# Kernel tuning notes

Measured on AMD Instinct MI355X. Metric: run time of the kernel, lower is better.

The kernel has to match this reference:

```python
import jax, jax.numpy as jnp
import numpy as np


def setup_inputs() -> dict:
    key = jax.random.key(0)
    kq, kk, kv = jax.random.split(key, 3)
    B, S, H, HK, D = 2, 2048, 32, 8, 128
    q = jax.random.normal(kq, (B, S, H, D), dtype=jnp.float32)
    k = jax.random.normal(kk, (B, S, HK, D), dtype=jnp.float32)
    v = jax.random.normal(kv, (B, S, HK, D), dtype=jnp.float32)
    return {"q": q, "k": k, "v": v}


def reference(q, k, v):
    # Causal grouped-query attention (the math vLLM's paged attention computes
    # for a full prefill where the KV cache holds exactly this sequence).
    B, S, H, D = q.shape
    HK = k.shape[2]
    G = H // HK  # query heads per kv head
    scale = jnp.asarray(D, q.dtype) ** -0.5
    qg = q.reshape(B, S, HK, G, D)
    # scores: [B, HK, G, S(q), S(k)]
    scores = jnp.einsum("bshgd,bthd->bhgst", qg, k) * scale
    causal = jnp.tril(jnp.ones((S, S), dtype=bool))  # [Sq, Sk]
    scores = jnp.where(causal, scores, jnp.finfo(scores.dtype).min)
    probs = jax.nn.softmax(scores, axis=-1)
    out = jnp.einsum("bhgst,bthd->bshgd", probs, v)  # [B, S, HK, G, D]
    return out.reshape(B, S, H * D)
```

## Files before the change

kernel.cpp:

```cpp
#include <hip/hip_runtime.h>
#include <hip/hip_bf16.h>

typedef __attribute__((ext_vector_type(8))) short short8;
typedef __attribute__((ext_vector_type(4))) short short4v;
typedef __attribute__((ext_vector_type(4))) float f32x4;
typedef __attribute__((ext_vector_type(16))) float f32x16;

#define MFMA32(a,b,c) __builtin_amdgcn_mfma_f32_32x32x16_bf16(a,b,c,0,0,0)

static __device__ __forceinline__ short f2bf(float f){
    union{float f;unsigned u;}x; x.f=f;
    unsigned r=(x.u+0x7FFFu+((x.u>>16)&1u))>>16;
    return (short)r;
}

static __device__ __forceinline__ unsigned pkbf(float lo, float hi){
    unsigned r;
    asm("v_cvt_pk_bf16_f32 %0, %1, %2" : "=v"(r) : "v"(lo), "v"(hi));
    return r;
}

static __device__ __forceinline__ void gl_lds16(const void* g, void* l){
    __builtin_amdgcn_global_load_lds(
        (const __attribute__((address_space(1))) unsigned int*)g,
        (__attribute__((address_space(3))) unsigned int*)l, 16, 0, 0);
}

static __device__ __forceinline__ short8 pfrag(int hi,
        float e0,float e1,float e2,float e3,
        float e4,float e5,float e6,float e7){
    unsigned a01 = pkbf(e0,e1), a23 = pkbf(e2,e3);
    unsigned a45 = pkbf(e4,e5), a67 = pkbf(e6,e7);
    unsigned b01 = __shfl_xor(a01, 32);
    unsigned b23 = __shfl_xor(a23, 32);
    unsigned b45 = __shfl_xor(a45, 32);
    unsigned b67 = __shfl_xor(a67, 32);
    union{ unsigned u[4]; short8 s; } w;
    w.u[0] = hi ? b45 : a01;
    w.u[1] = hi ? b67 : a23;
    w.u[2] = hi ? a45 : b01;
    w.u[3] = hi ? a67 : b23;
    return w.s;
}

constexpr int S_=2048, H_=32, HK_=8, D_=128;
constexpr int KVBLK=64;

__global__ __launch_bounds__(256) void prep(const float* __restrict__ k, const float* __restrict__ v,
                                            short* __restrict__ kb, short* __restrict__ vt){
    __shared__ short tile[64*65];
    int bid = blockIdx.x;
    if (bid < 4096){
        int t = bid*256 + threadIdx.x;
        int e = t*4;
        int d  = e & 127;
        int hk = (e>>7) & 7;
        int s  = (e>>10) & 2047;
        int b  = e>>21;
        f32x4 x = *(const f32x4*)(k + ((size_t)((b*S_+s)*HK_+hk))*D_ + d);
        short4v o;
        o[0]=f2bf(x[0]); o[1]=f2bf(x[1]); o[2]=f2bf(x[2]); o[3]=f2bf(x[3]);
        *(short4v*)(kb + ((size_t)((b*HK_+hk)*S_+s))*D_ + d) = o;
    } else {
        bid -= 4096;
        int d0 = (bid & 1)*64;
        int s0 = ((bid>>1) & 31)*64;
        int hk = (bid>>6) & 7;
        int b  = bid>>9;
        int tid = threadIdx.x;
        #pragma unroll
        for(int i=0;i<4;i++){
            int idx = i*1024 + tid*4;
            int r = idx>>6, c = idx&63;
            f32x4 x = *(const f32x4*)(v + ((size_t)((b*S_+s0+r)*HK_+hk))*D_ + d0 + c);
            tile[(c+0)*65 + r] = f2bf(x[0]);
            tile[(c+1)*65 + r] = f2bf(x[1]);
            tile[(c+2)*65 + r] = f2bf(x[2]);
            tile[(c+3)*65 + r] = f2bf(x[3]);
        }
        __syncthreads();
        #pragma unroll
        for(int i=0;i<4;i++){
            int idx = i*1024 + tid*4;
            int dr = idx>>6, c = idx&63;
            short4v o;
            o[0]=tile[dr*65+c]; o[1]=tile[dr*65+c+1]; o[2]=tile[dr*65+c+2]; o[3]=tile[dr*65+c+3];
            *(short4v*)(vt + ((size_t)((b*HK_+hk)*D_ + d0+dr))*S_ + s0 + c) = o;
        }
    }
}

__global__ __launch_bounds__(256,2) void attn_fwd(
    const float* __restrict__ q, const short* __restrict__ kb,
    const short* __restrict__ vtb, float* __restrict__ out)
{
    __shared__ __align__(16) unsigned char kls[KVBLK*D_*2];
    __shared__ __align__(16) unsigned char vls[D_*KVBLK*2];

    const int bid  = blockIdx.x;
    const int s    = bid >> 8;
    const int j    = bid & 255;
    const int xcd  = j & 7;
    const int t    = j >> 3;
    const int kvg  = xcd*2 + (t & 1);
    const int u    = t >> 1;
    const int hsub = u & 3;
    const int cq   = u >> 2;
    int c;
    switch(s){ case 0: c = 15-cq; break; case 1: c = 8+cq; break;
               case 2: c = 7-cq;  break; default: c = cq; }
    const int b    = kvg >> 3;
    const int hk   = kvg & 7;
    const int h    = hk*4 + hsub;
    const int q0   = c * 128;

    const int tid  = threadIdx.x;
    const int wave = tid >> 6;
    const int ln   = tid & 31;
    const int hi   = (tid >> 5) & 1;
    const int qg   = q0 + wave*32 + ln;

    const float qscale = 0.08838834764831845f * 1.4426950408889634f;

    const short* kt_base = kb  + (size_t)(b*HK_+hk)*S_*D_;
    const short* vt_base = vtb + (size_t)(b*HK_+hk)*D_*S_;

    short8 qf[8];
    {
        const float* qp = q + ((size_t)(b*S_ + qg)*H_ + h)*D_;
        #pragma unroll
        for(int kk=0;kk<8;kk++){
            int d0 = kk*16 + hi*8;
            f32x4 a = *(const f32x4*)(qp + d0);
            f32x4 cc= *(const f32x4*)(qp + d0 + 4);
            union{ unsigned u[4]; short8 s; } w;
            w.u[0]=pkbf(a[0]*qscale, a[1]*qscale);
            w.u[1]=pkbf(a[2]*qscale, a[3]*qscale);
            w.u[2]=pkbf(cc[0]*qscale, cc[1]*qscale);
            w.u[3]=pkbf(cc[2]*qscale, cc[3]*qscale);
            qf[kk]=w.s;
        }
    }

    f32x16 oac[4];
    #pragma unroll
    for(int dt=0;dt<4;dt++) oac[dt] = (f32x16)0.f;
    float m = -1e30f, l = 0.f;

    auto STAGE = [&](int kvt){
        const char* kg = (const char*)(kt_base + (size_t)kvt*KVBLK*D_);
        #pragma unroll
        for(int i=0;i<4;i++){
            int pp = (i*256 + tid)*16;
            int src = pp ^ (((pp>>8)&7)<<4);
            gl_lds16(kg + src, &kls[pp]);
        }
        const char* vg = (const char*)vt_base + (size_t)kvt*KVBLK*2;
        #pragma unroll
        for(int i=0;i<4;i++){
            int pp = (i*256 + tid)*16;
            int d = pp>>7;
            int src = (pp&127) ^ ((d&7)<<4);
            gl_lds16(vg + (size_t)d*(S_*2) + src, &vls[pp]);
        }
    };

    const int nkv    = 2*c + 2;
    const int kvmaxw = 2*c + (wave >> 1);

    for(int kvt=0; kvt<nkv; ++kvt){
        if (kvt) __syncthreads();
        STAGE(kvt);
        __syncthreads();

        if (kvt <= kvmaxw){
            const int kv0 = kvt*64;
            f32x16 sa0=(f32x16)0.f, sa1=(f32x16)0.f;
            const int sz = (ln&7)<<4;
            __builtin_amdgcn_s_setprio(1);
            #pragma unroll
            for(int kk=0;kk<8;kk++){
                int cb = kk*32 + hi*16;
                short8 k0 = *(const short8*)&kls[(ln*256 + cb) ^ sz];
                short8 k1 = *(const short8*)&kls[((ln+32)*256 + cb) ^ sz];
                sa0 = MFMA32(k0, qf[kk], sa0);
                sa1 = MFMA32(k1, qf[kk], sa1);
            }
            __builtin_amdgcn_s_setprio(0);
            if (kv0 + 63 > q0 + wave*32){
                #pragma unroll
                for(int r=0;r<16;r++){
                    int kvl = (r&3) + 8*(r>>2) + 4*hi;
                    if (kv0 + kvl      > qg) sa0[r] = -1e30f;
                    if (kv0 + 32 + kvl > qg) sa1[r] = -1e30f;
                }
            }
            float pm = sa0[0];
            #pragma unroll
            for(int r=1;r<16;r++) pm = fmaxf(pm, sa0[r]);
            #pragma unroll
            for(int r=0;r<16;r++) pm = fmaxf(pm, sa1[r]);
            pm = fmaxf(pm, __shfl_xor(pm, 32));
            if (!__all(pm <= m + 8.f)){
                float mn = fmaxf(m, pm);
                float sf = __builtin_amdgcn_exp2f(m - mn);
                m = mn; l *= sf;
                #pragma unroll
                for(int dt=0;dt<4;dt++){
                    #pragma unroll
                    for(int r=0;r<16;r++) oac[dt][r] *= sf;
                }
            }
            float ps = 0.f;
            #pragma unroll
            for(int r=0;r<16;r++){ sa0[r] = __builtin_amdgcn_exp2f(sa0[r]-m); ps += sa0[r]; }
            #pragma unroll
            for(int r=0;r<16;r++){ sa1[r] = __builtin_amdgcn_exp2f(sa1[r]-m); ps += sa1[r]; }
            l += ps + __shfl_xor(ps, 32);
            short8 pa0 = pfrag(hi, sa0[0],sa0[1],sa0[2], sa0[3], sa0[4], sa0[5], sa0[6], sa0[7]);
            short8 pa1 = pfrag(hi, sa0[8],sa0[9],sa0[10],sa0[11],sa0[12],sa0[13],sa0[14],sa0[15]);
            short8 pa2 = pfrag(hi, sa1[0],sa1[1],sa1[2], sa1[3], sa1[4], sa1[5], sa1[6], sa1[7]);
            short8 pa3 = pfrag(hi, sa1[8],sa1[9],sa1[10],sa1[11],sa1[12],sa1[13],sa1[14],sa1[15]);
            __builtin_amdgcn_s_setprio(1);
            #pragma unroll
            for(int dt=0;dt<4;dt++){
                int rb = (dt*32 + ln)*128;
                short8 v0 = *(const short8*)&vls[(rb +   0 + hi*16) ^ sz];
                oac[dt] = MFMA32(v0, pa0, oac[dt]);
                short8 v1 = *(const short8*)&vls[(rb +  32 + hi*16) ^ sz];
                oac[dt] = MFMA32(v1, pa1, oac[dt]);
                short8 v2 = *(const short8*)&vls[(rb +  64 + hi*16) ^ sz];
                oac[dt] = MFMA32(v2, pa2, oac[dt]);
                short8 v3 = *(const short8*)&vls[(rb +  96 + hi*16) ^ sz];
                oac[dt] = MFMA32(v3, pa3, oac[dt]);
            }
            __builtin_amdgcn_s_setprio(0);
        }
    }

    float rinv = 1.0f / l;
    float* op = out + ((size_t)(b*S_ + qg)*H_ + h)*D_;
    #pragma unroll
    for(int dt=0;dt<4;dt++){
        #pragma unroll
        for(int rr=0;rr<4;rr++){
            f32x4 o4;
            o4[0]=oac[dt][rr*4+0]*rinv;
            o4[1]=oac[dt][rr*4+1]*rinv;
            o4[2]=oac[dt][rr*4+2]*rinv;
            o4[3]=oac[dt][rr*4+3]*rinv;
            *(f32x4*)(op + dt*32 + rr*8 + hi*4) = o4;
        }
    }
}

extern "C" void kernel_launch(void* const* d_in, const int* in_sizes, int n_in,
                              void* d_out, int out_size, void* d_ws, size_t ws_size,
                              hipStream_t stream) {
    const float* q = (const float*)d_in[0];
    const float* k = (const float*)d_in[1];
    const float* v = (const float*)d_in[2];
    float* out = (float*)d_out;

    short* kb = (short*)d_ws;
    short* vt = (short*)((char*)d_ws + (size_t)2*HK_*S_*D_*2);

    prep<<<dim3(4096+1024), dim3(256), 0, stream>>>(k, v, kb, vt);
    attn_fwd<<<dim3(1024), dim3(256), 0, stream>>>(q, kb, vt, out);
}
```

Before: 118.7 us.

## Pre-swizzle K/V into MFMA fragment order and load directly from global

The prep kernel now writes K and V in bf16 laid out exactly in per-lane MFMA fragment order, so each lane fetches one contiguous 16-byte short8. The attention kernel drops the LDS staging and both block-level barriers and reads the fragments straight from global/L2. Each wave also stops at its own causal limit instead of following the block-wide loop. The cost is that the four waves no longer share one LDS copy, so each wave issues its own global reads, with more L2 traffic and exposed load latency and no explicit prefetch. The occupancy hint is also dropped from the launch bounds.

```diff
diff --git a/kernel.cpp b/kernel.cpp
--- a/kernel.cpp
+++ b/kernel.cpp
@@ -2,7 +2,6 @@
 #include <hip/hip_bf16.h>
 
 typedef __attribute__((ext_vector_type(8))) short short8;
-typedef __attribute__((ext_vector_type(4))) short short4v;
 typedef __attribute__((ext_vector_type(4))) float f32x4;
 typedef __attribute__((ext_vector_type(16))) float f32x16;
 
@@ -18,12 +17,6 @@
     unsigned r;
     asm("v_cvt_pk_bf16_f32 %0, %1, %2" : "=v"(r) : "v"(lo), "v"(hi));
     return r;
-}
-
-static __device__ __forceinline__ void gl_lds16(const void* g, void* l){
-    __builtin_amdgcn_global_load_lds(
-        (const __attribute__((address_space(1))) unsigned int*)g,
-        (__attribute__((address_space(3))) unsigned int*)l, 16, 0, 0);
 }
 
 static __device__ __forceinline__ short8 pfrag(int hi,
@@ -44,30 +37,37 @@
 }
 
 constexpr int S_=2048, H_=32, HK_=8, D_=128;
-constexpr int KVBLK=64;
+
 
 __global__ __launch_bounds__(256) void prep(const float* __restrict__ k, const float* __restrict__ v,
-                                            short* __restrict__ kb, short* __restrict__ vt){
+                                            short* __restrict__ kf, short* __restrict__ vf){
     __shared__ short tile[64*65];
     int bid = blockIdx.x;
-    if (bid < 4096){
-        int t = bid*256 + threadIdx.x;
-        int e = t*4;
-        int d  = e & 127;
-        int hk = (e>>7) & 7;
-        int s  = (e>>10) & 2047;
-        int b  = e>>21;
-        f32x4 x = *(const f32x4*)(k + ((size_t)((b*S_+s)*HK_+hk))*D_ + d);
-        short4v o;
-        o[0]=f2bf(x[0]); o[1]=f2bf(x[1]); o[2]=f2bf(x[2]); o[3]=f2bf(x[3]);
-        *(short4v*)(kb + ((size_t)((b*HK_+hk)*S_+s))*D_ + d) = o;
+    if (bid < 2048){
+        int gid = bid*256 + threadIdx.x;
+        int l   = gid & 63;
+        int hf  = (gid>>6)&1;
+        int kk  = (gid>>7)&7;
+        int T   = (gid>>10)&31;
+        int grp = gid>>15;
+        int b = grp>>3, hk = grp&7;
+        int row = T*64 + hf*32 + (l&31);
+        int e0  = kk*16 + (l>>5)*8;
+        const float* src = k + ((size_t)((b*S_+row)*HK_+hk))*D_ + e0;
+        f32x4 a = *(const f32x4*)src;
+        f32x4 c = *(const f32x4*)(src+4);
+        union{unsigned u[4]; short8 s;} w;
+        w.u[0]=pkbf(a[0],a[1]); w.u[1]=pkbf(a[2],a[3]);
+        w.u[2]=pkbf(c[0],c[1]); w.u[3]=pkbf(c[2],c[3]);
+        *(short8*)(kf + (size_t)gid*8) = w.s;
     } else {
-        bid -= 4096;
+        bid -= 2048;
         int d0 = (bid & 1)*64;
-        int s0 = ((bid>>1) & 31)*64;
-        int hk = (bid>>6) & 7;
+        int T  = (bid>>1)&31;
+        int hk = (bid>>6)&7;
         int b  = bid>>9;
         int tid = threadIdx.x;
+        int s0 = T*64;
         #pragma unroll
         for(int i=0;i<4;i++){
             int idx = i*1024 + tid*4;
@@ -79,24 +79,29 @@
             tile[(c+3)*65 + r] = f2bf(x[3]);
         }
         __syncthreads();
-        #pragma unroll
-        for(int i=0;i<4;i++){
-            int idx = i*1024 + tid*4;
-            int dr = idx>>6, c = idx&63;
-            short4v o;
-            o[0]=tile[dr*65+c]; o[1]=tile[dr*65+c+1]; o[2]=tile[dr*65+c+2]; o[3]=tile[dr*65+c+3];
-            *(short4v*)(vt + ((size_t)((b*HK_+hk)*D_ + d0+dr))*S_ + s0 + c) = o;
-        }
-    }
-}
-
-__global__ __launch_bounds__(256,2) void attn_fwd(
-    const float* __restrict__ q, const short* __restrict__ kb,
-    const short* __restrict__ vtb, float* __restrict__ out)
+        int grp = b*8 + hk;
+        #pragma unroll
+        for(int i=0;i<2;i++){
+            int slot = i*256 + tid;
+            int dtl = slot>>8;
+            int ks  = (slot>>6)&3;
+            int l   = slot&63;
+            int ddl = dtl*32 + (l&31);
+            int kvl = ks*16 + (l>>5)*8;
+            short8 o;
+            #pragma unroll
+            for(int j=0;j<8;j++) o[j] = tile[ddl*65 + kvl + j];
+            int dt = (d0>>5) + dtl;
+            size_t sg = ((((size_t)grp*32 + T)*4 + dt)*4 + ks)*64 + l;
+            *(short8*)(vf + sg*8) = o;
+        }
+    }
+}
+
+__global__ __launch_bounds__(256) void attn_fwd(
+    const float* __restrict__ q, const short* __restrict__ kf,
+    const short* __restrict__ vf, float* __restrict__ out)
 {
-    __shared__ __align__(16) unsigned char kls[KVBLK*D_*2];
-    __shared__ __align__(16) unsigned char vls[D_*KVBLK*2];
-
     const int bid  = blockIdx.x;
     const int s    = bid >> 8;
     const int j    = bid & 255;
@@ -116,14 +121,15 @@
 
     const int tid  = threadIdx.x;
     const int wave = tid >> 6;
+    const int lane = tid & 63;
     const int ln   = tid & 31;
     const int hi   = (tid >> 5) & 1;
     const int qg   = q0 + wave*32 + ln;
 
     const float qscale = 0.08838834764831845f * 1.4426950408889634f;
 
-    const short* kt_base = kb  + (size_t)(b*HK_+hk)*S_*D_;
-    const short* vt_base = vtb + (size_t)(b*HK_+hk)*D_*S_;
+    const short8* kfg = (const short8*)kf + ((size_t)kvg<<15);
+    const short8* vfg = (const short8*)vf + ((size_t)kvg<<15);
 
     short8 qf[8];
     {
@@ -147,95 +153,66 @@
     for(int dt=0;dt<4;dt++) oac[dt] = (f32x16)0.f;
     float m = -1e30f, l = 0.f;
 
-    auto STAGE = [&](int kvt){
-        const char* kg = (const char*)(kt_base + (size_t)kvt*KVBLK*D_);
-        #pragma unroll
-        for(int i=0;i<4;i++){
-            int pp = (i*256 + tid)*16;
-            int src = pp ^ (((pp>>8)&7)<<4);
-            gl_lds16(kg + src, &kls[pp]);
-        }
-        const char* vg = (const char*)vt_base + (size_t)kvt*KVBLK*2;
-        #pragma unroll
-        for(int i=0;i<4;i++){
-            int pp = (i*256 + tid)*16;
-            int d = pp>>7;
-            int src = (pp&127) ^ ((d&7)<<4);
-            gl_lds16(vg + (size_t)d*(S_*2) + src, &vls[pp]);
-        }
-    };
-
-    const int nkv    = 2*c + 2;
     const int kvmaxw = 2*c + (wave >> 1);
 
-    for(int kvt=0; kvt<nkv; ++kvt){
-        if (kvt) __syncthreads();
-        STAGE(kvt);
-        __syncthreads();
-
-        if (kvt <= kvmaxw){
-            const int kv0 = kvt*64;
-            f32x16 sa0=(f32x16)0.f, sa1=(f32x16)0.f;
-            const int sz = (ln&7)<<4;
-            __builtin_amdgcn_s_setprio(1);
+    for(int kvt=0; kvt<=kvmaxw; ++kvt){
+        const int kv0 = kvt*64;
+        const short8* kt = kfg + (size_t)kvt*1024;
+        const short8* vt = vfg + (size_t)kvt*1024;
+
+        f32x16 sa0=(f32x16)0.f, sa1=(f32x16)0.f;
+        __builtin_amdgcn_s_setprio(1);
+        #pragma unroll
+        for(int kk=0;kk<8;kk++){
+            short8 k0 = kt[(kk*2+0)*64 + lane];
+            short8 k1 = kt[(kk*2+1)*64 + lane];
+            sa0 = MFMA32(k0, qf[kk], sa0);
+            sa1 = MFMA32(k1, qf[kk], sa1);
+        }
+        __builtin_amdgcn_s_setprio(0);
+        if (kv0 + 63 > q0 + wave*32){
             #pragma unroll
-            for(int kk=0;kk<8;kk++){
-                int cb = kk*32 + hi*16;
-                short8 k0 = *(const short8*)&kls[(ln*256 + cb) ^ sz];
-                short8 k1 = *(const short8*)&kls[((ln+32)*256 + cb) ^ sz];
-                sa0 = MFMA32(k0, qf[kk], sa0);
-                sa1 = MFMA32(k1, qf[kk], sa1);
+            for(int r=0;r<16;r++){
+                int kvl = (r&3) + 8*(r>>2) + 4*hi;
+                if (kv0 + kvl      > qg) sa0[r] = -1e30f;
+                if (kv0 + 32 + kvl > qg) sa1[r] = -1e30f;
             }
-            __builtin_amdgcn_s_setprio(0);
-            if (kv0 + 63 > q0 + wave*32){
-                #pragma unroll
-                for(int r=0;r<16;r++){
-                    int kvl = (r&3) + 8*(r>>2) + 4*hi;
-                    if (kv0 + kvl      > qg) sa0[r] = -1e30f;
-                    if (kv0 + 32 + kvl > qg) sa1[r] = -1e30f;
-                }
-            }
-            float pm = sa0[0];
-            #pragma unroll
-            for(int r=1;r<16;r++) pm = fmaxf(pm, sa0[r]);
-            #pragma unroll
-            for(int r=0;r<16;r++) pm = fmaxf(pm, sa1[r]);
-            pm = fmaxf(pm, __shfl_xor(pm, 32));
-            if (!__all(pm <= m + 8.f)){
-                float mn = fmaxf(m, pm);
-                float sf = __builtin_amdgcn_exp2f(m - mn);
-                m = mn; l *= sf;
-                #pragma unroll
-                for(int dt=0;dt<4;dt++){
-                    #pragma unroll
-                    for(int r=0;r<16;r++) oac[dt][r] *= sf;
-                }
-            }
-            float ps = 0.f;
-            #pragma unroll
-            for(int r=0;r<16;r++){ sa0[r] = __builtin_amdgcn_exp2f(sa0[r]-m); ps += sa0[r]; }
-            #pragma unroll
-            for(int r=0;r<16;r++){ sa1[r] = __builtin_amdgcn_exp2f(sa1[r]-m); ps += sa1[r]; }
-            l += ps + __shfl_xor(ps, 32);
-            short8 pa0 = pfrag(hi, sa0[0],sa0[1],sa0[2], sa0[3], sa0[4], sa0[5], sa0[6], sa0[7]);
-            short8 pa1 = pfrag(hi, sa0[8],sa0[9],sa0[10],sa0[11],sa0[12],sa0[13],sa0[14],sa0[15]);
-            short8 pa2 = pfrag(hi, sa1[0],sa1[1],sa1[2], sa1[3], sa1[4], sa1[5], sa1[6], sa1[7]);
-            short8 pa3 = pfrag(hi, sa1[8],sa1[9],sa1[10],sa1[11],sa1[12],sa1[13],sa1[14],sa1[15]);
-            __builtin_amdgcn_s_setprio(1);
+        }
+        float pm = sa0[0];
+        #pragma unroll
+        for(int r=1;r<16;r++) pm = fmaxf(pm, sa0[r]);
+        #pragma unroll
+        for(int r=0;r<16;r++) pm = fmaxf(pm, sa1[r]);
+        pm = fmaxf(pm, __shfl_xor(pm, 32));
+        if (!__all(pm <= m + 8.f)){
+            float mn = fmaxf(m, pm);
+            float sf = __builtin_amdgcn_exp2f(m - mn);
+            m = mn; l *= sf;
             #pragma unroll
             for(int dt=0;dt<4;dt++){
-                int rb = (dt*32 + ln)*128;
-                short8 v0 = *(const short8*)&vls[(rb +   0 + hi*16) ^ sz];
-                oac[dt] = MFMA32(v0, pa0, oac[dt]);
-                short8 v1 = *(const short8*)&vls[(rb +  32 + hi*16) ^ sz];
-                oac[dt] = MFMA32(v1, pa1, oac[dt]);
-                short8 v2 = *(const short8*)&vls[(rb +  64 + hi*16) ^ sz];
-                oac[dt] = MFMA32(v2, pa2, oac[dt]);
-                short8 v3 = *(const short8*)&vls[(rb +  96 + hi*16) ^ sz];
-                oac[dt] = MFMA32(v3, pa3, oac[dt]);
+                #pragma unroll
+                for(int r=0;r<16;r++) oac[dt][r] *= sf;
             }
-            __builtin_amdgcn_s_setprio(0);
-        }
+        }
+        float ps = 0.f;
+        #pragma unroll
+        for(int r=0;r<16;r++){ sa0[r] = __builtin_amdgcn_exp2f(sa0[r]-m); ps += sa0[r]; }
+        #pragma unroll
+        for(int r=0;r<16;r++){ sa1[r] = __builtin_amdgcn_exp2f(sa1[r]-m); ps += sa1[r]; }
+        l += ps + __shfl_xor(ps, 32);
+        short8 pa0 = pfrag(hi, sa0[0],sa0[1],sa0[2], sa0[3], sa0[4], sa0[5], sa0[6], sa0[7]);
+        short8 pa1 = pfrag(hi, sa0[8],sa0[9],sa0[10],sa0[11],sa0[12],sa0[13],sa0[14],sa0[15]);
+        short8 pa2 = pfrag(hi, sa1[0],sa1[1],sa1[2], sa1[3], sa1[4], sa1[5], sa1[6], sa1[7]);
+        short8 pa3 = pfrag(hi, sa1[8],sa1[9],sa1[10],sa1[11],sa1[12],sa1[13],sa1[14],sa1[15]);
+        __builtin_amdgcn_s_setprio(1);
+        #pragma unroll
+        for(int dt=0;dt<4;dt++){
+            oac[dt] = MFMA32(vt[(dt*4+0)*64 + lane], pa0, oac[dt]);
+            oac[dt] = MFMA32(vt[(dt*4+1)*64 + lane], pa1, oac[dt]);
+            oac[dt] = MFMA32(vt[(dt*4+2)*64 + lane], pa2, oac[dt]);
+            oac[dt] = MFMA32(vt[(dt*4+3)*64 + lane], pa3, oac[dt]);
+        }
+        __builtin_amdgcn_s_setprio(0);
     }
 
     float rinv = 1.0f / l;
@@ -262,9 +239,9 @@
     const float* v = (const float*)d_in[2];
     float* out = (float*)d_out;
 
-    short* kb = (short*)d_ws;
-    short* vt = (short*)((char*)d_ws + (size_t)2*HK_*S_*D_*2);
-
-    prep<<<dim3(4096+1024), dim3(256), 0, stream>>>(k, v, kb, vt);
-    attn_fwd<<<dim3(1024), dim3(256), 0, stream>>>(q, kb, vt, out);
-}
+    short* kf = (short*)d_ws;
+    short* vf = (short*)((char*)d_ws + (size_t)8*1024*1024);
+
+    prep<<<dim3(2048+1024), dim3(256), 0, stream>>>(k, v, kf, vf);
+    attn_fwd<<<dim3(1024), dim3(256), 0, stream>>>(q, kf, vf, out);
+}
```

Measured after the change: 197.8 us. +66.7%, slower.
